# Performance work log

Hardware: AMD Instinct MI355X
Metric: run time of the kernel (lower is better)

The kernel has to match this reference:

```python
import jax, jax.numpy as jnp
import numpy as np

N, E, F, H, G, C = 50000, 600000, 128, 128, 500, 10
BN_EPS = 1e-5

def setup_inputs() -> dict:
    key = jax.random.key(0)
    ks = jax.random.split(key, 20)
    def lin(k, fan_in, shape):
        b = 1.0 / np.sqrt(fan_in)
        return jax.random.uniform(k, shape, jnp.float32, -b, b)
    inp = {
        'x': jax.random.normal(ks[0], (N, F), jnp.float32),
        'edge_index': jax.random.randint(ks[1], (2, E), 0, N, jnp.int64),
        'batch': jnp.sort(jax.random.randint(ks[2], (N,), 0, G, jnp.int64)),
        # conv1 MLP: Linear(F,H) -> BN(H) -> ReLU -> Dropout -> Linear(H,H) -> ReLU
        'W1a': lin(ks[3], F, (F, H)), 'b1a': lin(ks[4], F, (H,)),
        'g1': jnp.ones((H,), jnp.float32), 'be1': jnp.zeros((H,), jnp.float32),
        'm1': jnp.zeros((H,), jnp.float32), 'v1': jnp.ones((H,), jnp.float32),
        'W1b': lin(ks[5], H, (H, H)), 'b1b': lin(ks[6], H, (H,)),
        # conv2 MLP: Linear(H,H) -> ReLU -> BN(H) -> Dropout -> Linear(H,H) -> ReLU
        'W2a': lin(ks[7], H, (H, H)), 'b2a': lin(ks[8], H, (H,)),
        'g2': jnp.ones((H,), jnp.float32), 'be2': jnp.zeros((H,), jnp.float32),
        'm2': jnp.zeros((H,), jnp.float32), 'v2': jnp.ones((H,), jnp.float32),
        'W2b': lin(ks[9], H, (H, H)), 'b2b': lin(ks[10], H, (H,)),
        # heads
        'Wl1': lin(ks[11], 2 * H, (2 * H, H // 2)), 'bl1': lin(ks[12], 2 * H, (H // 2,)),
        'Wl2': lin(ks[13], H // 2, (H // 2, C)), 'bl2': lin(ks[14], H // 2, (C,)),
    }
    return inp

def _bn(h, g, b, m, v):
    return (h - m) * (g / jnp.sqrt(v + BN_EPS)) + b

def _gin_aggregate(x, src, dst):
    # out[i] = x[i] + sum_{j->i} x[j]  (GINConv with eps=0)
    return x + jax.ops.segment_sum(x[src], dst, num_segments=N)

def reference(x, edge_index, batch,
              W1a, b1a, g1, be1, m1, v1, W1b, b1b,
              W2a, b2a, g2, be2, m2, v2, W2b, b2b,
              Wl1, bl1, Wl2, bl2):
    src, dst = edge_index[0], edge_index[1]
    # conv1
    a1 = _gin_aggregate(x, src, dst)                       # [N, F]
    h1 = _bn(a1 @ W1a + b1a, g1, be1, m1, v1)
    h1 = jax.nn.relu(h1)                                   # dropout = identity (eval)
    h1 = jax.nn.relu(h1 @ W1b + b1b)                       # [N, H]
    # conv2
    a2 = _gin_aggregate(h1, src, dst)                      # [N, H]
    h2 = jax.nn.relu(a2 @ W2a + b2a)
    h2 = _bn(h2, g2, be2, m2, v2)
    h2 = jax.nn.relu(h2 @ W2b + b2b)                       # [N, H]
    # global add pool per graph
    p1 = jax.ops.segment_sum(h1, batch, num_segments=G)    # [G, H]
    p2 = jax.ops.segment_sum(h2, batch, num_segments=G)    # [G, H]
    z = jnp.concatenate((p1, p2), axis=1)                  # [G, 2H]
    z = jax.nn.relu(z @ Wl1 + bl1)
    return z @ Wl2 + bl2                                   # [G, C]
```

## Files before the change

kernel.cpp:

```cpp
#include <hip/hip_runtime.h>

#define N_NODES 50000
#define N_EDGES 600000
#define HDIM 128
#define NGRAPH 500
#define NCLASS 10
#define BN_EPS 1e-5f
#define KSLOT 64

typedef short short8 __attribute__((ext_vector_type(8)));
typedef float floatx4 __attribute__((ext_vector_type(4)));

__device__ __forceinline__ float bf2f(unsigned short u) {
    unsigned int v = ((unsigned int)u) << 16;
    return __uint_as_float(v);
}
__device__ __forceinline__ unsigned short f2bf(float f) {
    unsigned int u = __float_as_uint(f);
    unsigned int r = (u + 0x7fffu + ((u >> 16) & 1u)) >> 16;
    return (unsigned short)r;
}

#define NB_CAST 6250
#define NB_ZERO 196
#define NB_PREPW 256
#define NB_SETUP (NB_CAST + NB_ZERO + NB_PREPW + 1)

__global__ void k_setup(const float* __restrict__ x, unsigned short* __restrict__ xb,
                        int* __restrict__ cnt,
                        const float* __restrict__ W1a, const float* __restrict__ W1b,
                        const float* __restrict__ W2a, const float* __restrict__ W2b,
                        unsigned short* __restrict__ wpack,
                        const float* __restrict__ b1a, const float* __restrict__ g1,
                        const float* __restrict__ be1, const float* __restrict__ m1,
                        const float* __restrict__ v1, const float* __restrict__ b1b,
                        const float* __restrict__ b2a, const float* __restrict__ g2,
                        const float* __restrict__ be2, const float* __restrict__ m2,
                        const float* __restrict__ v2, const float* __restrict__ b2b,
                        float* __restrict__ ep) {
    int b = blockIdx.x;
    int t = threadIdx.x;
    if (b < NB_CAST) {
        int i = b * 256 + t;
        float4 v = ((const float4*)x)[i];
        ushort4 o;
        o.x = f2bf(v.x); o.y = f2bf(v.y); o.z = f2bf(v.z); o.w = f2bf(v.w);
        ((ushort4*)xb)[i] = o;
        return;
    }
    b -= NB_CAST;
    if (b < NB_ZERO) {
        int i = b * 256 + t;
        if (i < N_NODES) cnt[i] = 0;
        return;
    }
    b -= NB_ZERO;
    if (b < NB_PREPW) {
        int e = b * 256 + t;
        int w = e >> 14;
        int s_ = e & 16383;
        int j = s_ & 7;
        int m = (s_ >> 3) & 15;
        int q = (s_ >> 7) & 3;
        int ks = (s_ >> 9) & 3;
        int ct = (s_ >> 11) & 7;
        int n = ct * 16 + m;
        int k;
        float scale = 1.f;
        if (w == 0 || w == 2) {
            k = ks * 32 + q * 8 + j;
        } else {
            k = (ks * 2 + (j >> 2)) * 16 + q * 4 + (j & 3);
            if (w == 3) scale = g2[k] * rsqrtf(v2[k] + BN_EPS);
        }
        const float* W = (w == 0) ? W1a : (w == 1) ? W1b : (w == 2) ? W2a : W2b;
        wpack[e] = f2bf(W[k * 128 + n] * scale);
        return;
    }
    if (t < 128) {
        int j = t;
        float s1 = g1[j] * rsqrtf(v1[j] + BN_EPS);
        ep[0 * 256 + 0 + j]   = s1;
        ep[0 * 256 + 128 + j] = (b1a[j] - m1[j]) * s1 + be1[j];
        ep[1 * 256 + 0 + j]   = 1.f;
        ep[1 * 256 + 128 + j] = b2a[j];
        ep[512 + j] = b1b[j];
        float acc = b2b[j];
        for (int k = 0; k < 128; k++) {
            float s2k = g2[k] * rsqrtf(v2[k] + BN_EPS);
            acc += (be2[k] - m2[k] * s2k) * W2b[k * 128 + j];
        }
        ep[512 + 128 + j] = acc;
    }
}

__global__ void k_scatter(const int* __restrict__ src, const int* __restrict__ dst,
                          int* __restrict__ cnt, int* __restrict__ adj, int e) {
    int i = blockIdx.x * blockDim.x + threadIdx.x;
    if (i < e) {
        int d = dst[i];
        int p = atomicAdd(&cnt[d], 1);
        if (p < KSLOT) adj[d * KSLOT + p] = src[i];
    }
}

__global__ __launch_bounds__(256, 4) void k_conv(const unsigned short* __restrict__ A,
                                                 const int* __restrict__ cnt,
                                                 const int* __restrict__ adj,
                                                 const unsigned short* __restrict__ WaP,
                                                 const unsigned short* __restrict__ WbP,
                                                 const float* __restrict__ epi,
                                                 const float* __restrict__ epf,
                                                 unsigned short* __restrict__ Out, int n) {
    int t = threadIdx.x;
    int lane = t & 63;
    int w = t >> 6;
    int q = lane >> 4;
    int m = lane & 15;

    int base = blockIdx.x * 64 + w * 16;
    int node = base + m;
    if (node >= n) node = n - 1;

    float acc[4][8];
    #pragma unroll
    for (int s = 0; s < 4; s++) {
        short8 sv = *(const short8*)(A + (size_t)node * 128 + s * 32 + q * 8);
        #pragma unroll
        for (int j = 0; j < 8; j++) acc[s][j] = bf2f((unsigned short)sv[j]);
    }
    {
        int len = cnt[node];
        if (len > KSLOT) len = KSLOT;
        const int* ad = adj + node * KSLOT;
        int i = 0;
        for (; i + 4 <= len; i += 4) {
            int u0 = ad[i], u1 = ad[i + 1], u2 = ad[i + 2], u3 = ad[i + 3];
            short8 f0[4], f1[4], f2[4], f3[4];
            #pragma unroll
            for (int s = 0; s < 4; s++) {
                f0[s] = *(const short8*)(A + (size_t)u0 * 128 + s * 32 + q * 8);
                f1[s] = *(const short8*)(A + (size_t)u1 * 128 + s * 32 + q * 8);
                f2[s] = *(const short8*)(A + (size_t)u2 * 128 + s * 32 + q * 8);
                f3[s] = *(const short8*)(A + (size_t)u3 * 128 + s * 32 + q * 8);
            }
            #pragma unroll
            for (int s = 0; s < 4; s++)
                #pragma unroll
                for (int j = 0; j < 8; j++)
                    acc[s][j] += bf2f((unsigned short)f0[s][j]) + bf2f((unsigned short)f1[s][j]) +
                                 bf2f((unsigned short)f2[s][j]) + bf2f((unsigned short)f3[s][j]);
        }
        if (i + 2 <= len) {
            int u0 = ad[i], u1 = ad[i + 1];
            short8 f0[4], f1[4];
            #pragma unroll
            for (int s = 0; s < 4; s++) {
                f0[s] = *(const short8*)(A + (size_t)u0 * 128 + s * 32 + q * 8);
                f1[s] = *(const short8*)(A + (size_t)u1 * 128 + s * 32 + q * 8);
            }
            #pragma unroll
            for (int s = 0; s < 4; s++)
                #pragma unroll
                for (int j = 0; j < 8; j++)
                    acc[s][j] += bf2f((unsigned short)f0[s][j]) + bf2f((unsigned short)f1[s][j]);
            i += 2;
        }
        if (i < len) {
            int u0 = ad[i];
            #pragma unroll
            for (int s = 0; s < 4; s++) {
                short8 f0 = *(const short8*)(A + (size_t)u0 * 128 + s * 32 + q * 8);
                #pragma unroll
                for (int j = 0; j < 8; j++) acc[s][j] += bf2f((unsigned short)f0[j]);
            }
        }
    }
    short8 a1[4];
    #pragma unroll
    for (int s = 0; s < 4; s++)
        #pragma unroll
        for (int j = 0; j < 8; j++) a1[s][j] = (short)f2bf(acc[s][j]);

    int lbase = lane * 8;

    floatx4 acc1[8];
    #pragma unroll
    for (int c = 0; c < 8; c++) acc1[c] = (floatx4)0.f;
    #pragma unroll
    for (int s = 0; s < 4; s++) {
        #pragma unroll
        for (int ct = 0; ct < 8; ct++) {
            short8 wf = *(const short8*)(WaP + (ct * 4 + s) * 512 + lbase);
            acc1[ct] = __builtin_amdgcn_mfma_f32_16x16x32_bf16(wf, a1[s], acc1[ct], 0, 0, 0);
        }
    }

    short8 a2[4];
    #pragma unroll
    for (int s = 0; s < 4; s++) {
        #pragma unroll
        for (int j = 0; j < 8; j++) {
            int ct = s * 2 + (j >> 2);
            int r = j & 3;
            int col = ct * 16 + q * 4 + r;
            float P = epi[col], Q = epi[128 + col];
            float v = fmaxf(fmaf(acc1[ct][r], P, Q), 0.f);
            a2[s][j] = (short)f2bf(v);
        }
    }

    floatx4 acc2[8];
    #pragma unroll
    for (int c = 0; c < 8; c++) acc2[c] = (floatx4)0.f;
    #pragma unroll
    for (int s = 0; s < 4; s++) {
        #pragma unroll
        for (int ct = 0; ct < 8; ct++) {
            short8 wf = *(const short8*)(WbP + (ct * 4 + s) * 512 + lbase);
            acc2[ct] = __builtin_amdgcn_mfma_f32_16x16x32_bf16(a2[s], wf, acc2[ct], 0, 0, 0);
        }
    }

    #pragma unroll
    for (int ct = 0; ct < 8; ct++) {
        int col = ct * 16 + m;
        float Qf = epf[col];
        #pragma unroll
        for (int r = 0; r < 4; r++) {
            int gr = base + q * 4 + r;
            if (gr < n)
                Out[(size_t)gr * 128 + col] = f2bf(fmaxf(acc2[ct][r] + Qf, 0.f));
        }
    }
}

__global__ void k_pool_head(const unsigned short* __restrict__ h1, const unsigned short* __restrict__ h2,
                            const int* __restrict__ batch, const float* __restrict__ Wl1,
                            const float* __restrict__ bl1, const float* __restrict__ Wl2,
                            const float* __restrict__ bl2, float* __restrict__ out) {
    int g = blockIdx.x;
    int t = threadIdx.x;
    int lo = 0, hi = N_NODES;
    while (lo < hi) { int mid = (lo + hi) >> 1; if (batch[mid] < g) lo = mid + 1; else hi = mid; }
    int start = lo;
    lo = 0; hi = N_NODES;
    while (lo < hi) { int mid = (lo + hi) >> 1; if (batch[mid] < g + 1) lo = mid + 1; else hi = mid; }
    int end = lo;

    int w = t >> 6, l = t & 63;
    const unsigned int* h = (w < 2) ? (const unsigned int*)h1 : (const unsigned int*)h2;
    int sub = w & 1;
    float ax = 0.f, ay = 0.f;
    int i = start + sub;
    for (; i + 6 < end; i += 8) {
        unsigned int v0 = h[(size_t)(i + 0) * 64 + l];
        unsigned int v1 = h[(size_t)(i + 2) * 64 + l];
        unsigned int v2 = h[(size_t)(i + 4) * 64 + l];
        unsigned int v3 = h[(size_t)(i + 6) * 64 + l];
        ax += bf2f((unsigned short)(v0 & 0xffff)) + bf2f((unsigned short)(v1 & 0xffff)) +
              bf2f((unsigned short)(v2 & 0xffff)) + bf2f((unsigned short)(v3 & 0xffff));
        ay += bf2f((unsigned short)(v0 >> 16)) + bf2f((unsigned short)(v1 >> 16)) +
              bf2f((unsigned short)(v2 >> 16)) + bf2f((unsigned short)(v3 >> 16));
    }
    for (; i < end; i += 2) {
        unsigned int v0 = h[(size_t)i * 64 + l];
        ax += bf2f((unsigned short)(v0 & 0xffff));
        ay += bf2f((unsigned short)(v0 >> 16));
    }

    __shared__ float red[4][128];
    __shared__ float zin[256];
    __shared__ float zmid[64];
    red[w][2 * l] = ax;
    red[w][2 * l + 1] = ay;
    __syncthreads();
    int mat = t >> 7, col = t & 127;
    zin[t] = red[mat * 2][col] + red[mat * 2 + 1][col];
    __syncthreads();
    if (t < 64) {
        float acc = bl1[t];
        #pragma unroll 8
        for (int k = 0; k < 256; k++) acc = fmaf(zin[k], Wl1[k * 64 + t], acc);
        zmid[t] = fmaxf(acc, 0.f);
    }
    __syncthreads();
    if (t < NCLASS) {
        float acc = bl2[t];
        #pragma unroll
        for (int j = 0; j < 64; j++) acc = fmaf(zmid[j], Wl2[j * 10 + t], acc);
        out[g * NCLASS + t] = acc;
    }
}


extern "C" void kernel_launch(void* const* d_in, const int* in_sizes, int n_in,
                              void* d_out, int out_size, void* d_ws, size_t ws_size,
                              hipStream_t stream) {
    const float* x   = (const float*)d_in[0];
    const int* eidx  = (const int*)d_in[1];
    const int* batch = (const int*)d_in[2];
    const float* W1a = (const float*)d_in[3];
    const float* b1a = (const float*)d_in[4];
    const float* g1  = (const float*)d_in[5];
    const float* be1 = (const float*)d_in[6];
    const float* m1  = (const float*)d_in[7];
    const float* v1  = (const float*)d_in[8];
    const float* W1b = (const float*)d_in[9];
    const float* b1b = (const float*)d_in[10];
    const float* W2a = (const float*)d_in[11];
    const float* b2a = (const float*)d_in[12];
    const float* g2  = (const float*)d_in[13];
    const float* be2 = (const float*)d_in[14];
    const float* m2  = (const float*)d_in[15];
    const float* v2  = (const float*)d_in[16];
    const float* W2b = (const float*)d_in[17];
    const float* b2b = (const float*)d_in[18];
    const float* Wl1 = (const float*)d_in[19];
    const float* bl1 = (const float*)d_in[20];
    const float* Wl2 = (const float*)d_in[21];
    const float* bl2 = (const float*)d_in[22];
    const int* srcv = eidx;
    const int* dstv = eidx + N_EDGES;

    char* ws = (char*)d_ws;
    size_t off = 0;
    auto alloc = [&](size_t bytes) -> void* {
        void* p = ws + off;
        off = (off + bytes + 255) & ~(size_t)255;
        return p;
    };
    int* cnt      = (int*)alloc(sizeof(int) * N_NODES);
    int* adj      = (int*)alloc(sizeof(int) * (size_t)N_NODES * KSLOT);
    float* ep     = (float*)alloc(sizeof(float) * 768);
    unsigned short* wpack = (unsigned short*)alloc(sizeof(unsigned short) * 4 * 16384);
    unsigned short* xb    = (unsigned short*)alloc(sizeof(unsigned short) * (size_t)N_NODES * HDIM);
    unsigned short* bufB  = (unsigned short*)alloc(sizeof(unsigned short) * (size_t)N_NODES * HDIM);
    unsigned short* bufC  = (unsigned short*)alloc(sizeof(unsigned short) * (size_t)N_NODES * HDIM);
    (void)ws_size; (void)in_sizes; (void)n_in; (void)out_size;

    float* outp = (float*)d_out;

    k_setup<<<dim3(NB_SETUP), dim3(256), 0, stream>>>(
        x, xb, cnt, W1a, W1b, W2a, W2b, wpack,
        b1a, g1, be1, m1, v1, b1b, b2a, g2, be2, m2, v2, b2b, ep);
    k_scatter<<<dim3((N_EDGES + 255) / 256), dim3(256), 0, stream>>>(srcv, dstv, cnt, adj, N_EDGES);

    dim3 cgrid((N_NODES + 63) / 64), cblk(256);
    k_conv<<<cgrid, cblk, 0, stream>>>(xb, cnt, adj, wpack + 0 * 16384, wpack + 1 * 16384,
                                       ep + 0, ep + 512, bufC, N_NODES);
    k_conv<<<cgrid, cblk, 0, stream>>>(bufC, cnt, adj, wpack + 2 * 16384, wpack + 3 * 16384,
                                       ep + 256, ep + 640, bufB, N_NODES);
    k_pool_head<<<dim3(NGRAPH), dim3(256), 0, stream>>>(bufC, bufB, batch, Wl1, bl1, Wl2, bl2, outp);
}
```

Before: 264.1 us.

## Split neighbor aggregation of each 16-node tile across four waves with LDS reduction

Each block now handles 16 nodes instead of 64. The four waves split each node's neighbor list by stride and sum their partial results through shared memory. The goal is more memory-level parallelism per node and a shorter per-wave gather chain, which should hide gather latency better. In exchange, all four waves redundantly run the full MFMA MLP for the same 16 rows, each writing only a quarter of the output columns, so matrix and weight-load work goes up fourfold. A block barrier and 36KB of LDS are also added, which may limit occupancy.

```diff
diff --git a/kernel.cpp b/kernel.cpp
--- a/kernel.cpp
+++ b/kernel.cpp
@@ -112,47 +112,38 @@
                                                  const float* __restrict__ epi,
                                                  const float* __restrict__ epf,
                                                  unsigned short* __restrict__ Out, int n) {
+    __shared__ float part[4][64][36];
     int t = threadIdx.x;
     int lane = t & 63;
-    int w = t >> 6;
+    int wv = t >> 6;
     int q = lane >> 4;
     int m = lane & 15;
 
-    int base = blockIdx.x * 64 + w * 16;
+    int base = blockIdx.x * 16;
     int node = base + m;
     if (node >= n) node = n - 1;
 
     float acc[4][8];
-    #pragma unroll
-    for (int s = 0; s < 4; s++) {
-        short8 sv = *(const short8*)(A + (size_t)node * 128 + s * 32 + q * 8);
-        #pragma unroll
-        for (int j = 0; j < 8; j++) acc[s][j] = bf2f((unsigned short)sv[j]);
+    if (wv == 0) {
+        #pragma unroll
+        for (int s = 0; s < 4; s++) {
+            short8 sv = *(const short8*)(A + (size_t)node * 128 + s * 32 + q * 8);
+            #pragma unroll
+            for (int j = 0; j < 8; j++) acc[s][j] = bf2f((unsigned short)sv[j]);
+        }
+    } else {
+        #pragma unroll
+        for (int s = 0; s < 4; s++)
+            #pragma unroll
+            for (int j = 0; j < 8; j++) acc[s][j] = 0.f;
     }
     {
         int len = cnt[node];
         if (len > KSLOT) len = KSLOT;
         const int* ad = adj + node * KSLOT;
-        int i = 0;
-        for (; i + 4 <= len; i += 4) {
-            int u0 = ad[i], u1 = ad[i + 1], u2 = ad[i + 2], u3 = ad[i + 3];
-            short8 f0[4], f1[4], f2[4], f3[4];
-            #pragma unroll
-            for (int s = 0; s < 4; s++) {
-                f0[s] = *(const short8*)(A + (size_t)u0 * 128 + s * 32 + q * 8);
-                f1[s] = *(const short8*)(A + (size_t)u1 * 128 + s * 32 + q * 8);
-                f2[s] = *(const short8*)(A + (size_t)u2 * 128 + s * 32 + q * 8);
-                f3[s] = *(const short8*)(A + (size_t)u3 * 128 + s * 32 + q * 8);
-            }
-            #pragma unroll
-            for (int s = 0; s < 4; s++)
-                #pragma unroll
-                for (int j = 0; j < 8; j++)
-                    acc[s][j] += bf2f((unsigned short)f0[s][j]) + bf2f((unsigned short)f1[s][j]) +
-                                 bf2f((unsigned short)f2[s][j]) + bf2f((unsigned short)f3[s][j]);
-        }
-        if (i + 2 <= len) {
-            int u0 = ad[i], u1 = ad[i + 1];
+        int i = wv;
+        for (; i + 4 < len; i += 8) {
+            int u0 = ad[i], u1 = ad[i + 4];
             short8 f0[4], f1[4];
             #pragma unroll
             for (int s = 0; s < 4; s++) {
@@ -164,7 +155,6 @@
                 #pragma unroll
                 for (int j = 0; j < 8; j++)
                     acc[s][j] += bf2f((unsigned short)f0[s][j]) + bf2f((unsigned short)f1[s][j]);
-            i += 2;
         }
         if (i < len) {
             int u0 = ad[i];
@@ -174,6 +164,24 @@
                 #pragma unroll
                 for (int j = 0; j < 8; j++) acc[s][j] += bf2f((unsigned short)f0[j]);
             }
+        }
+    }
+    #pragma unroll
+    for (int c = 0; c < 8; c++)
+        *(float4*)(&part[wv][lane][c * 4]) =
+            make_float4(acc[c >> 1][(c & 1) * 4 + 0], acc[c >> 1][(c & 1) * 4 + 1],
+                        acc[c >> 1][(c & 1) * 4 + 2], acc[c >> 1][(c & 1) * 4 + 3]);
+    __syncthreads();
+    #pragma unroll
+    for (int ow = 1; ow < 4; ow++) {
+        int o = (wv + ow) & 3;
+        #pragma unroll
+        for (int c = 0; c < 8; c++) {
+            float4 v = *(const float4*)(&part[o][lane][c * 4]);
+            acc[c >> 1][(c & 1) * 4 + 0] += v.x;
+            acc[c >> 1][(c & 1) * 4 + 1] += v.y;
+            acc[c >> 1][(c & 1) * 4 + 2] += v.z;
+            acc[c >> 1][(c & 1) * 4 + 3] += v.w;
         }
     }
     short8 a1[4];
@@ -223,7 +231,8 @@
     }
 
     #pragma unroll
-    for (int ct = 0; ct < 8; ct++) {
+    for (int cti = 0; cti < 2; cti++) {
+        int ct = wv * 2 + cti;
         int col = ct * 16 + m;
         float Qf = epf[col];
         #pragma unroll
@@ -346,7 +355,7 @@
         b1a, g1, be1, m1, v1, b1b, b2a, g2, be2, m2, v2, b2b, ep);
     k_scatter<<<dim3((N_EDGES + 255) / 256), dim3(256), 0, stream>>>(srcv, dstv, cnt, adj, N_EDGES);
 
-    dim3 cgrid((N_NODES + 63) / 64), cblk(256);
+    dim3 cgrid((N_NODES + 15) / 16), cblk(256);
     k_conv<<<cgrid, cblk, 0, stream>>>(xb, cnt, adj, wpack + 0 * 16384, wpack + 1 * 16384,
                                        ep + 0, ep + 512, bufC, N_NODES);
     k_conv<<<cgrid, cblk, 0, stream>>>(bufC, cnt, adj, wpack + 2 * 16384, wpack + 3 * 16384,
```

Measured after the change: 313.1 us. 1.19x slower.

## Split fused gather-MLP conv into separate aggregation and MFMA MLP kernels

Applied to the files above, without the earlier changes.

The fused conv kernel, which gathered neighbour rows and then ran the MFMA MLP, is split into two kernels. The new k_agg kernel gives each node 16 threads, each loading one 16-byte chunk, unrolls the neighbour loop by 8 and reads the adjacency list with int4 loads. This is meant to expose more memory-level parallelism for the irregular gather, free from the register pressure and occupancy limits of the MFMA kernel. The cost is an extra round-trip of the aggregated bf16 feature matrix through global memory for each layer, plus two extra kernel launches.

```diff
diff --git a/kernel.cpp b/kernel.cpp
--- a/kernel.cpp
+++ b/kernel.cpp
@@ -104,14 +104,84 @@
     }
 }
 
-__global__ __launch_bounds__(256, 4) void k_conv(const unsigned short* __restrict__ A,
-                                                 const int* __restrict__ cnt,
-                                                 const int* __restrict__ adj,
-                                                 const unsigned short* __restrict__ WaP,
-                                                 const unsigned short* __restrict__ WbP,
-                                                 const float* __restrict__ epi,
-                                                 const float* __restrict__ epf,
-                                                 unsigned short* __restrict__ Out, int n) {
+__global__ __launch_bounds__(256) void k_agg(const unsigned short* __restrict__ x,
+                                             const int* __restrict__ cnt,
+                                             const int* __restrict__ adj,
+                                             unsigned short* __restrict__ out) {
+    int g = blockIdx.x * 256 + threadIdx.x;
+    int node = g >> 4;
+    int m = g & 15;
+    if (node >= N_NODES) return;
+
+    float acc[8];
+    {
+        short8 self = *(const short8*)(x + (size_t)node * 128 + m * 8);
+        #pragma unroll
+        for (int j = 0; j < 8; j++) acc[j] = bf2f((unsigned short)self[j]);
+    }
+    int len = cnt[node];
+    if (len > KSLOT) len = KSLOT;
+    const int* ad = adj + node * KSLOT;
+    int i = 0;
+    for (; i + 8 <= len; i += 8) {
+        int4 ua = *(const int4*)(ad + i);
+        int4 ub = *(const int4*)(ad + i + 4);
+        short8 f0 = *(const short8*)(x + (size_t)ua.x * 128 + m * 8);
+        short8 f1 = *(const short8*)(x + (size_t)ua.y * 128 + m * 8);
+        short8 f2 = *(const short8*)(x + (size_t)ua.z * 128 + m * 8);
+        short8 f3 = *(const short8*)(x + (size_t)ua.w * 128 + m * 8);
+        short8 f4 = *(const short8*)(x + (size_t)ub.x * 128 + m * 8);
+        short8 f5 = *(const short8*)(x + (size_t)ub.y * 128 + m * 8);
+        short8 f6 = *(const short8*)(x + (size_t)ub.z * 128 + m * 8);
+        short8 f7 = *(const short8*)(x + (size_t)ub.w * 128 + m * 8);
+        #pragma unroll
+        for (int j = 0; j < 8; j++) {
+            float a = bf2f((unsigned short)f0[j]) + bf2f((unsigned short)f1[j]) +
+                      bf2f((unsigned short)f2[j]) + bf2f((unsigned short)f3[j]);
+            float b = bf2f((unsigned short)f4[j]) + bf2f((unsigned short)f5[j]) +
+                      bf2f((unsigned short)f6[j]) + bf2f((unsigned short)f7[j]);
+            acc[j] += a + b;
+        }
+    }
+    if (i + 4 <= len) {
+        int4 ua = *(const int4*)(ad + i);
+        short8 f0 = *(const short8*)(x + (size_t)ua.x * 128 + m * 8);
+        short8 f1 = *(const short8*)(x + (size_t)ua.y * 128 + m * 8);
+        short8 f2 = *(const short8*)(x + (size_t)ua.z * 128 + m * 8);
+        short8 f3 = *(const short8*)(x + (size_t)ua.w * 128 + m * 8);
+        #pragma unroll
+        for (int j = 0; j < 8; j++)
+            acc[j] += bf2f((unsigned short)f0[j]) + bf2f((unsigned short)f1[j]) +
+                      bf2f((unsigned short)f2[j]) + bf2f((unsigned short)f3[j]);
+        i += 4;
+    }
+    if (i + 2 <= len) {
+        int u0 = ad[i], u1 = ad[i + 1];
+        short8 f0 = *(const short8*)(x + (size_t)u0 * 128 + m * 8);
+        short8 f1 = *(const short8*)(x + (size_t)u1 * 128 + m * 8);
+        #pragma unroll
+        for (int j = 0; j < 8; j++)
+            acc[j] += bf2f((unsigned short)f0[j]) + bf2f((unsigned short)f1[j]);
+        i += 2;
+    }
+    if (i < len) {
+        int u0 = ad[i];
+        short8 f0 = *(const short8*)(x + (size_t)u0 * 128 + m * 8);
+        #pragma unroll
+        for (int j = 0; j < 8; j++) acc[j] += bf2f((unsigned short)f0[j]);
+    }
+    short8 r;
+    #pragma unroll
+    for (int j = 0; j < 8; j++) r[j] = (short)f2bf(acc[j]);
+    *(short8*)(out + (size_t)node * 128 + m * 8) = r;
+}
+
+__global__ __launch_bounds__(256, 4) void k_mlp(const unsigned short* __restrict__ A,
+                                                const unsigned short* __restrict__ WaP,
+                                                const unsigned short* __restrict__ WbP,
+                                                const float* __restrict__ epi,
+                                                const float* __restrict__ epf,
+                                                unsigned short* __restrict__ Out, int n) {
     int t = threadIdx.x;
     int lane = t & 63;
     int w = t >> 6;
@@ -122,65 +192,10 @@
     int node = base + m;
     if (node >= n) node = n - 1;
 
-    float acc[4][8];
-    #pragma unroll
-    for (int s = 0; s < 4; s++) {
-        short8 sv = *(const short8*)(A + (size_t)node * 128 + s * 32 + q * 8);
-        #pragma unroll
-        for (int j = 0; j < 8; j++) acc[s][j] = bf2f((unsigned short)sv[j]);
-    }
-    {
-        int len = cnt[node];
-        if (len > KSLOT) len = KSLOT;
-        const int* ad = adj + node * KSLOT;
-        int i = 0;
-        for (; i + 4 <= len; i += 4) {
-            int u0 = ad[i], u1 = ad[i + 1], u2 = ad[i + 2], u3 = ad[i + 3];
-            short8 f0[4], f1[4], f2[4], f3[4];
-            #pragma unroll
-            for (int s = 0; s < 4; s++) {
-                f0[s] = *(const short8*)(A + (size_t)u0 * 128 + s * 32 + q * 8);
-                f1[s] = *(const short8*)(A + (size_t)u1 * 128 + s * 32 + q * 8);
-                f2[s] = *(const short8*)(A + (size_t)u2 * 128 + s * 32 + q * 8);
-                f3[s] = *(const short8*)(A + (size_t)u3 * 128 + s * 32 + q * 8);
-            }
-            #pragma unroll
-            for (int s = 0; s < 4; s++)
-                #pragma unroll
-                for (int j = 0; j < 8; j++)
-                    acc[s][j] += bf2f((unsigned short)f0[s][j]) + bf2f((unsigned short)f1[s][j]) +
-                                 bf2f((unsigned short)f2[s][j]) + bf2f((unsigned short)f3[s][j]);
-        }
-        if (i + 2 <= len) {
-            int u0 = ad[i], u1 = ad[i + 1];
-            short8 f0[4], f1[4];
-            #pragma unroll
-            for (int s = 0; s < 4; s++) {
-                f0[s] = *(const short8*)(A + (size_t)u0 * 128 + s * 32 + q * 8);
-                f1[s] = *(const short8*)(A + (size_t)u1 * 128 + s * 32 + q * 8);
-            }
-            #pragma unroll
-            for (int s = 0; s < 4; s++)
-                #pragma unroll
-                for (int j = 0; j < 8; j++)
-                    acc[s][j] += bf2f((unsigned short)f0[s][j]) + bf2f((unsigned short)f1[s][j]);
-            i += 2;
-        }
-        if (i < len) {
-            int u0 = ad[i];
-            #pragma unroll
-            for (int s = 0; s < 4; s++) {
-                short8 f0 = *(const short8*)(A + (size_t)u0 * 128 + s * 32 + q * 8);
-                #pragma unroll
-                for (int j = 0; j < 8; j++) acc[s][j] += bf2f((unsigned short)f0[j]);
-            }
-        }
-    }
     short8 a1[4];
     #pragma unroll
     for (int s = 0; s < 4; s++)
-        #pragma unroll
-        for (int j = 0; j < 8; j++) a1[s][j] = (short)f2bf(acc[s][j]);
+        a1[s] = *(const short8*)(A + (size_t)node * 128 + s * 32 + q * 8);
 
     int lbase = lane * 8;
 
@@ -335,6 +350,7 @@
     float* ep     = (float*)alloc(sizeof(float) * 768);
     unsigned short* wpack = (unsigned short*)alloc(sizeof(unsigned short) * 4 * 16384);
     unsigned short* xb    = (unsigned short*)alloc(sizeof(unsigned short) * (size_t)N_NODES * HDIM);
+    unsigned short* bufA  = (unsigned short*)alloc(sizeof(unsigned short) * (size_t)N_NODES * HDIM);
     unsigned short* bufB  = (unsigned short*)alloc(sizeof(unsigned short) * (size_t)N_NODES * HDIM);
     unsigned short* bufC  = (unsigned short*)alloc(sizeof(unsigned short) * (size_t)N_NODES * HDIM);
     (void)ws_size; (void)in_sizes; (void)n_in; (void)out_size;
@@ -346,10 +362,14 @@
         b1a, g1, be1, m1, v1, b1b, b2a, g2, be2, m2, v2, b2b, ep);
     k_scatter<<<dim3((N_EDGES + 255) / 256), dim3(256), 0, stream>>>(srcv, dstv, cnt, adj, N_EDGES);
 
-    dim3 cgrid((N_NODES + 63) / 64), cblk(256);
-    k_conv<<<cgrid, cblk, 0, stream>>>(xb, cnt, adj, wpack + 0 * 16384, wpack + 1 * 16384,
-                                       ep + 0, ep + 512, bufC, N_NODES);
-    k_conv<<<cgrid, cblk, 0, stream>>>(bufC, cnt, adj, wpack + 2 * 16384, wpack + 3 * 16384,
-                                       ep + 256, ep + 640, bufB, N_NODES);
+    dim3 agrid((N_NODES * 16 + 255) / 256), ablk(256);
+    dim3 mgrid((N_NODES + 63) / 64), mblk(256);
+
+    k_agg<<<agrid, ablk, 0, stream>>>(xb, cnt, adj, bufA);
+    k_mlp<<<mgrid, mblk, 0, stream>>>(bufA, wpack + 0 * 16384, wpack + 1 * 16384,
+                                      ep + 0, ep + 512, bufC, N_NODES);
+    k_agg<<<agrid, ablk, 0, stream>>>(bufC, cnt, adj, bufA);
+    k_mlp<<<mgrid, mblk, 0, stream>>>(bufA, wpack + 2 * 16384, wpack + 3 * 16384,
+                                      ep + 256, ep + 640, bufB, N_NODES);
     k_pool_head<<<dim3(NGRAPH), dim3(256), 0, stream>>>(bufC, bufB, batch, Wl1, bl1, Wl2, bl2, outp);
 }
```

Result: no change. 261.3 us (-1.1%).
